# Kernel optimization log

Measured on AMD Instinct MI355X. Metric: run time of the kernel, lower is better.

The kernel has to match this reference:

```python
import jax, jax.numpy as jnp
import numpy as np

N_NODES = 100000
N_EDGES = 1600000
F_IN = 100
HEADS = 3
HEAD_DIM = 64
HIDDEN = HEADS * HEAD_DIM  # 192
NUM_GRAPHS = 128
NUM_CLASSES = 2
NEG_SLOPE_ATT = 0.2   # PyG GATConv attention leaky_relu slope
NEG_SLOPE_ACT = 0.01  # F.leaky_relu default slope


def setup_inputs() -> dict:
    key = jax.random.key(0)
    ks = jax.random.split(key, 9)
    x = jax.random.normal(ks[0], (N_NODES, F_IN), dtype=jnp.float32)
    edge_index = jax.random.randint(ks[1], (2, N_EDGES), 0, N_NODES, dtype=jnp.int64)
    batch = jnp.sort(jax.random.randint(ks[2], (N_NODES,), 0, NUM_GRAPHS, dtype=jnp.int64))
    s = 0.05
    W = jax.random.normal(ks[3], (F_IN, HIDDEN), dtype=jnp.float32) * s
    att_src = jax.random.normal(ks[4], (HEADS, HEAD_DIM), dtype=jnp.float32) * s
    att_dst = jax.random.normal(ks[5], (HEADS, HEAD_DIM), dtype=jnp.float32) * s
    bias = jax.random.normal(ks[6], (HIDDEN,), dtype=jnp.float32) * s
    cls_W = jax.random.normal(ks[7], (HIDDEN, NUM_CLASSES), dtype=jnp.float32) * s
    cls_b = jax.random.normal(ks[8], (NUM_CLASSES,), dtype=jnp.float32) * s
    return {"x": x, "edge_index": edge_index, "batch": batch, "W": W,
            "att_src": att_src, "att_dst": att_dst, "bias": bias,
            "cls_W": cls_W, "cls_b": cls_b}


def _gat_forward(x, edge_index, batch, W, att_src, att_dst, bias, cls_W, cls_b):
    N = x.shape[0]
    # PyG GATConv adds self-loops by default
    loops = jnp.arange(N, dtype=edge_index.dtype)
    src = jnp.concatenate([edge_index[0], loops])
    dst = jnp.concatenate([edge_index[1], loops])

    h = (x @ W).reshape(N, HEADS, HEAD_DIM)          # [N,H,C]
    a_src = jnp.sum(h * att_src, axis=-1)            # [N,H]
    a_dst = jnp.sum(h * att_dst, axis=-1)            # [N,H]

    e = a_src[src] + a_dst[dst]                      # [Etot,H]
    e = jax.nn.leaky_relu(e, NEG_SLOPE_ATT)

    # segment softmax over incoming edges of each destination node
    m = jax.ops.segment_max(e, dst, num_segments=N)  # [N,H]
    e = jnp.exp(e - m[dst])
    denom = jax.ops.segment_sum(e, dst, num_segments=N)
    alpha = e / denom[dst]                           # [Etot,H]

    msg = h[src] * alpha[:, :, None]                 # [Etot,H,C]
    out = jax.ops.segment_sum(msg, dst, num_segments=N).reshape(N, HIDDEN) + bias

    out = jax.nn.leaky_relu(out, NEG_SLOPE_ACT)      # F.leaky_relu (dropout inactive: eval)
    pooled = jax.ops.segment_max(out, batch, num_segments=NUM_GRAPHS)  # global_max_pool
    return pooled @ cls_W + cls_b                    # [NUM_GRAPHS, NUM_CLASSES]


def reference(x, edge_index, batch, W, att_src, att_dst, bias, cls_W, cls_b):
    return _gat_forward(x, edge_index, batch, W, att_src, att_dst, bias, cls_W, cls_b)
```

## Files before the change

kernel.cpp:

```cpp
#include <hip/hip_runtime.h>
#include <math.h>

#define N_NODES   100000
#define N_EDGES   1600000
#define ETOT      1700000
#define F_IN      100
#define HEADS     3
#define HEAD_DIM  64
#define HIDDEN    192
#define NUM_GRAPHS 128
#define NUM_CLASSES 2
#define WT_COLS   208
#define KPAD      128
#define NCHUNK    ((ETOT + 1023) / 1024)
#define DRANGE    (N_NODES / 8)
#define NGEMM     (N_NODES / 32)
#define SCAT_BLKS 2048
#define OSTRIDE   200
#define GAGG      16
#define CAP       64

typedef unsigned short ushort_t;
typedef __attribute__((ext_vector_type(8))) short short8;
typedef __attribute__((ext_vector_type(4))) float floatx4;

__device__ __forceinline__ unsigned f2ord(float f) {
    unsigned u = __float_as_uint(f);
    return (u & 0x80000000u) ? ~u : (u | 0x80000000u);
}
__device__ __forceinline__ float ord2f(unsigned u) {
    return __uint_as_float((u & 0x80000000u) ? (u & 0x7fffffffu) : ~u);
}
__device__ __forceinline__ unsigned bf16rn(float f) {
    unsigned u = __float_as_uint(f);
    return (u + 0x7fffu + ((u >> 16) & 1u)) >> 16;
}
__device__ __forceinline__ int rl_i(int v, int l) {
    return __builtin_amdgcn_readlane(v, l);
}
__device__ __forceinline__ float rl_f(float v, int l) {
    return __uint_as_float((unsigned)__builtin_amdgcn_readlane((int)__float_as_uint(v), l));
}
template<int CTRL>
__device__ __forceinline__ float bfly(float v) {
    int t = __builtin_amdgcn_update_dpp(0, (int)__float_as_uint(v), CTRL, 0xF, 0xF, false);
    return v + __uint_as_float((unsigned)t);
}
#define DPP_XOR1 0xB1
#define DPP_XOR2 0x4E
#define DPP_XOR8 0x128

__global__ __launch_bounds__(256) void k_prep(
        const float* __restrict__ W, const float* __restrict__ att_src,
        const float* __restrict__ att_dst,
        ushort_t* __restrict__ WT_hi, ushort_t* __restrict__ WT_lo) {
    const int c0 = blockIdx.x * 8;
    const int t = threadIdx.x;
    __shared__ float wsv_s[F_IN * 6];
    if (c0 < HIDDEN + 6 && c0 + 8 > HIDDEN) {
        for (int p = t; p < F_IN * 6; p += 256) {
            int k = p / 6, j = p % 6;
            const float* a = (j < 3) ? att_src : att_dst;
            int hh = j % 3;
            float s = 0.f;
            for (int c = 0; c < HEAD_DIM; c++)
                s += W[k * HIDDEN + hh * HEAD_DIM + c] * a[hh * HEAD_DIM + c];
            wsv_s[p] = s;
        }
        __syncthreads();
    }
    for (int idx = t; idx < 8 * KPAD; idx += 256) {
        int col = c0 + (idx >> 7), k = idx & (KPAD - 1);
        float v = 0.f;
        if (k < F_IN) {
            if (col < HIDDEN) v = W[k * HIDDEN + col];
            else if (col < HIDDEN + 6) v = wsv_s[k * 6 + (col - HIDDEN)];
        }
        unsigned hi = bf16rn(v);
        WT_hi[col * KPAD + k] = (ushort_t)hi;
        float lo = v - __uint_as_float(hi << 16);
        WT_lo[col * KPAD + k] = (ushort_t)bf16rn(lo);
    }
}

__global__ __launch_bounds__(256) void k_gemm(
        const float* __restrict__ x,
        const ushort_t* __restrict__ WT_hi, const ushort_t* __restrict__ WT_lo,
        ushort_t* __restrict__ hb,
        float* __restrict__ asrc, float* __restrict__ adst) {
    __shared__ ushort_t lds[32 * 136 * 2];
    const int tid = threadIdx.x;

    ushort_t* xs_hi = lds;
    ushort_t* xs_lo = lds + 32 * 136;
    const int base = blockIdx.x * 32;
    for (int idx = tid; idx < 32 * 14; idx += 256) {
        int row = idx / 14, u = idx % 14;
        *(unsigned*)(xs_hi + row * 136 + 100 + u * 2) = 0u;
        *(unsigned*)(xs_lo + row * 136 + 100 + u * 2) = 0u;
    }
    for (int p = tid; p < 32 * 25; p += 256) {
        int row = p / 25, q = p % 25;
        float4 v = *(const float4*)(x + (size_t)(base + row) * F_IN + q * 4);
        float vv[4] = {v.x, v.y, v.z, v.w};
        ushort_t h4[4], l4[4];
#pragma unroll
        for (int e = 0; e < 4; e++) {
            unsigned hi = bf16rn(vv[e]);
            h4[e] = (ushort_t)hi;
            float lo = vv[e] - __uint_as_float(hi << 16);
            l4[e] = (ushort_t)bf16rn(lo);
        }
        int off = row * 136 + q * 4;
        *(uint2*)(xs_hi + off) = *(uint2*)h4;
        *(uint2*)(xs_lo + off) = *(uint2*)l4;
    }
    __syncthreads();

    const int wid = tid >> 6, l = tid & 63;
    const int row16 = l & 15, g = l >> 4;
    const int NT = (wid == 3) ? 4 : 3;
    const int t0 = wid * 3;

    floatx4 acc[2][4];
#pragma unroll
    for (int m = 0; m < 2; m++)
#pragma unroll
        for (int i = 0; i < 4; i++) acc[m][i] = (floatx4)0.f;

#pragma unroll
    for (int c = 0; c < 4; c++) {
        const int ke = g * 8 + c * 32;
        short8 ah0 = *(const short8*)(xs_hi + row16 * 136 + ke);
        short8 al0 = *(const short8*)(xs_lo + row16 * 136 + ke);
        short8 ah1 = *(const short8*)(xs_hi + (16 + row16) * 136 + ke);
        short8 al1 = *(const short8*)(xs_lo + (16 + row16) * 136 + ke);
#pragma unroll
        for (int ti = 0; ti < 4; ti++) {
            if (ti >= NT) break;
            const int col = (t0 + ti) * 16 + row16;
            short8 bh = *(const short8*)(WT_hi + col * KPAD + ke);
            short8 bl = *(const short8*)(WT_lo + col * KPAD + ke);
            acc[0][ti] = __builtin_amdgcn_mfma_f32_16x16x32_bf16(ah0, bh, acc[0][ti], 0, 0, 0);
            acc[0][ti] = __builtin_amdgcn_mfma_f32_16x16x32_bf16(ah0, bl, acc[0][ti], 0, 0, 0);
            acc[0][ti] = __builtin_amdgcn_mfma_f32_16x16x32_bf16(al0, bh, acc[0][ti], 0, 0, 0);
            acc[1][ti] = __builtin_amdgcn_mfma_f32_16x16x32_bf16(ah1, bh, acc[1][ti], 0, 0, 0);
            acc[1][ti] = __builtin_amdgcn_mfma_f32_16x16x32_bf16(ah1, bl, acc[1][ti], 0, 0, 0);
            acc[1][ti] = __builtin_amdgcn_mfma_f32_16x16x32_bf16(al1, bh, acc[1][ti], 0, 0, 0);
        }
    }

    __syncthreads();

#pragma unroll
    for (int ti = 0; ti < 4; ti++) {
        if (ti >= NT) break;
        const int tile = t0 + ti;
        if (tile < 12) {
#pragma unroll
            for (int m = 0; m < 2; m++)
#pragma unroll
                for (int r = 0; r < 4; r++) {
                    int node = m * 16 + g * 4 + r;
                    lds[node * OSTRIDE + tile * 16 + row16] =
                        (ushort_t)bf16rn(acc[m][ti][r]);
                }
        } else if (row16 < 6) {
#pragma unroll
            for (int m = 0; m < 2; m++)
#pragma unroll
                for (int r = 0; r < 4; r++) {
                    int node = base + m * 16 + g * 4 + r;
                    if (row16 < 3) asrc[node * HEADS + row16] = acc[m][ti][r];
                    else           adst[node * HEADS + (row16 - 3)] = acc[m][ti][r];
                }
        }
    }
    __syncthreads();

    uint4* hb4 = (uint4*)(hb + (size_t)base * HIDDEN);
#pragma unroll
    for (int i = 0; i < 3; i++) {
        int q = tid + i * 256;
        int row = q / 24, c8 = q % 24;
        hb4[q] = *(const uint4*)(lds + row * OSTRIDE + c8 * 8);
    }
}

__global__ __launch_bounds__(256) void k_scat(
        const int* __restrict__ ei, int* __restrict__ count,
        int* __restrict__ srcs) {
    const int tid = threadIdx.x;
    const int s = blockIdx.x;
    const int cls = s & 7;
    const int dlo = cls * DRANGE, dhi = dlo + DRANGE;
    for (int chunk = s >> 3; chunk < NCHUNK; chunk += SCAT_BLKS / 8) {
        const int base = chunk * 1024 + tid;
        int d4[4], s4[4];
#pragma unroll
        for (int q = 0; q < 4; q++) {
            int j = base + q * 256;
            if (j >= ETOT) { d4[q] = -1; s4[q] = 0; continue; }
            d4[q] = (j < N_EDGES) ? ei[N_EDGES + j] : (j - N_EDGES);
            s4[q] = (j < N_EDGES) ? ei[j] : d4[q];
        }
#pragma unroll
        for (int q = 0; q < 4; q++) {
            int d = d4[q];
            if (d < dlo || d >= dhi) continue;
            int pos = atomicAdd(&count[d], 1);
            if (pos < CAP) srcs[d * CAP + pos] = s4[q];
        }
    }
}

__global__ __launch_bounds__(192) void k_aggr(const int* __restrict__ count,
        const int* __restrict__ srcs, const float* __restrict__ asrc,
        const float* __restrict__ adst, const ushort_t* __restrict__ hb,
        const float* __restrict__ bias, const int* __restrict__ batch,
        unsigned* __restrict__ pooled) {
    __shared__ float sm[HIDDEN];
    const int n0 = blockIdx.x * GAGG;
    const int tid = threadIdx.x;
    const int head = tid >> 6, lane = tid & 63;
    const int srci = (lane & 3) | ((lane >> 1) & 4);
    const int slot = ((lane >> 2) & 1) | ((lane >> 3) & 6);
    const char* hbase = (const char*)hb + head * 128 + slot * 16;
    const int c0 = head * HEAD_DIM + slot * 8;

    int cntv = (lane < GAGG) ? count[n0 + lane] : 0;
    int bgv  = (lane < GAGG) ? batch[n0 + lane] : 0;
    float adv = (lane < GAGG * HEADS) ? adst[n0 * HEADS + lane] : 0.f;
    float bv[8];
#pragma unroll
    for (int k = 0; k < 8; k++) bv[k] = bias[c0 + k];

    float vmax[8];
#pragma unroll
    for (int k = 0; k < 8; k++) vmax[k] = -INFINITY;
    int curg = rl_i(bgv, 0);

    int cnt_cur = rl_i(cntv, 0); if (cnt_cur > CAP) cnt_cur = CAP;
    int sA = srcs[(size_t)n0 * CAP + lane];
    int sB = (GAGG > 1) ? srcs[(size_t)(n0 + 1) * CAP + lane] : 0;
    float aA = (lane < cnt_cur) ? asrc[sA * HEADS + head] : 0.f;

    for (int g = 0; g < GAGG; g++) {
        const int gg = rl_i(bgv, g);
        if (gg != curg) {
            if ((lane & 11) == 0) {
#pragma unroll
                for (int k = 0; k < 8; k++) sm[c0 + k] = vmax[k];
            }
            __syncthreads();
            atomicMax(&pooled[curg * HIDDEN + tid], f2ord(sm[tid]));
            __syncthreads();
#pragma unroll
            for (int k = 0; k < 8; k++) vmax[k] = -INFINITY;
            curg = gg;
        }

        const int cnt = cnt_cur;
        const float ad = rl_f(adv, g * HEADS + head);

        int sC = (g + 2 < GAGG) ? srcs[(size_t)(n0 + g + 2) * CAP + lane] : 0;
        int cnt_nxt = 0; float aB = 0.f;
        if (g + 1 < GAGG) {
            cnt_nxt = rl_i(cntv, g + 1); if (cnt_nxt > CAP) cnt_nxt = CAP;
            if (lane < cnt_nxt) aB = asrc[sB * HEADS + head];
        }

        float myexp = 0.f; int myoff = 0;
        if (lane < cnt) {
            float e = aA + ad;
            e = (e > 0.f) ? e : 0.2f * e;
            myexp = __expf(e);
            myoff = sA * (HIDDEN * 2);
        }

        float acc[8];
#pragma unroll
        for (int k = 0; k < 8; k++) acc[k] = 0.f;
        float dpart = 0.f;
        int groups = (cnt + 7) >> 3;
#pragma unroll 2
        for (int j = 0; j < groups; j++) {
            int sl = j * 8 + srci;
            float a   = __shfl(myexp, sl);
            int   off = __shfl(myoff, sl);
            uint4 u = *(const uint4*)(hbase + off);
            acc[0] += a * __uint_as_float(u.x << 16);
            acc[1] += a * __uint_as_float(u.x & 0xffff0000u);
            acc[2] += a * __uint_as_float(u.y << 16);
            acc[3] += a * __uint_as_float(u.y & 0xffff0000u);
            acc[4] += a * __uint_as_float(u.z << 16);
            acc[5] += a * __uint_as_float(u.z & 0xffff0000u);
            acc[6] += a * __uint_as_float(u.w << 16);
            acc[7] += a * __uint_as_float(u.w & 0xffff0000u);
            dpart += a;
        }

        dpart = bfly<DPP_XOR1>(dpart);
        dpart = bfly<DPP_XOR2>(dpart);
        dpart = bfly<DPP_XOR8>(dpart);
#pragma unroll
        for (int k = 0; k < 8; k++) {
            acc[k] = bfly<DPP_XOR1>(acc[k]);
            acc[k] = bfly<DPP_XOR2>(acc[k]);
            acc[k] = bfly<DPP_XOR8>(acc[k]);
        }

        const float inv = 1.f / dpart;
#pragma unroll
        for (int k = 0; k < 8; k++) {
            float v = acc[k] * inv + bv[k];
            v = (v > 0.f) ? v : 0.01f * v;
            vmax[k] = fmaxf(vmax[k], v);
        }

        sA = sB; sB = sC; aA = aB; cnt_cur = cnt_nxt;
    }

    if ((lane & 11) == 0) {
#pragma unroll
        for (int k = 0; k < 8; k++) sm[c0 + k] = vmax[k];
    }
    __syncthreads();
    atomicMax(&pooled[curg * HIDDEN + tid], f2ord(sm[tid]));
}

__global__ __launch_bounds__(64) void k_cls(const unsigned* __restrict__ pooled,
        const float* __restrict__ clsW, const float* __restrict__ clsb,
        float* __restrict__ out) {
    const int g = blockIdx.x, lane = threadIdx.x;
    float s0 = 0.f, s1 = 0.f;
#pragma unroll
    for (int i = 0; i < 3; i++) {
        int f = i * 64 + lane;
        float pv = ord2f(pooled[g * HIDDEN + f]);
        s0 += pv * clsW[f * NUM_CLASSES];
        s1 += pv * clsW[f * NUM_CLASSES + 1];
    }
#pragma unroll
    for (int m = 1; m < 64; m <<= 1) {
        s0 += __shfl_xor(s0, m);
        s1 += __shfl_xor(s1, m);
    }
    if (lane == 0) {
        out[g * NUM_CLASSES]     = s0 + clsb[0];
        out[g * NUM_CLASSES + 1] = s1 + clsb[1];
    }
}

extern "C" void kernel_launch(void* const* d_in, const int* in_sizes, int n_in,
                              void* d_out, int out_size, void* d_ws, size_t ws_size,
                              hipStream_t stream) {
    const float* x       = (const float*)d_in[0];
    const int*   ei      = (const int*)d_in[1];
    const int*   batch   = (const int*)d_in[2];
    const float* W       = (const float*)d_in[3];
    const float* att_src = (const float*)d_in[4];
    const float* att_dst = (const float*)d_in[5];
    const float* bias    = (const float*)d_in[6];
    const float* clsW    = (const float*)d_in[7];
    const float* clsb    = (const float*)d_in[8];
    float* out = (float*)d_out;

    char* p = (char*)d_ws;
    auto alloc = [&](size_t bytes) {
        char* r = p; p += (bytes + 255) & ~size_t(255); return r;
    };
    ushort_t* hb     = (ushort_t*)alloc(sizeof(ushort_t) * N_NODES * HIDDEN);
    float*    asrc   = (float*)   alloc(sizeof(float) * N_NODES * HEADS);
    float*    adst   = (float*)   alloc(sizeof(float) * N_NODES * HEADS);
    int*      count  = (int*)     alloc(sizeof(int) * N_NODES);
    int*      srcs   = (int*)     alloc(sizeof(int) * (size_t)N_NODES * CAP);
    ushort_t* WT_hi  = (ushort_t*)alloc(sizeof(ushort_t) * WT_COLS * KPAD);
    ushort_t* WT_lo  = (ushort_t*)alloc(sizeof(ushort_t) * WT_COLS * KPAD);
    unsigned* pooled = (unsigned*)alloc(sizeof(unsigned) * NUM_GRAPHS * HIDDEN);

    hipMemsetAsync(count, 0, sizeof(int) * N_NODES, stream);
    hipMemsetAsync(pooled, 0, sizeof(unsigned) * NUM_GRAPHS * HIDDEN, stream);

    k_prep<<<WT_COLS / 8, 256, 0, stream>>>(W, att_src, att_dst, WT_hi, WT_lo);
    k_gemm<<<NGEMM, 256, 0, stream>>>(x, WT_hi, WT_lo, hb, asrc, adst);
    k_scat<<<SCAT_BLKS, 256, 0, stream>>>(ei, count, srcs);
    k_aggr<<<N_NODES / GAGG, 192, 0, stream>>>(count, srcs, asrc, adst, hb, bias,
                                               batch, pooled);
    k_cls<<<NUM_GRAPHS, 64, 0, stream>>>(pooled, clsW, clsb, out);
}
```

Measured before the change: 359.1 us.

## Merge edge scatter and GEMM into one launch, batch aggregation gathers

The GEMM and the edge-bucketing scatter are merged into one kernel, with the first blocks doing the scatter and the rest doing the GEMM, so the two independent stages can overlap on the GPU and one launch is saved. Scatter stores and aggregation loads of the source lists now use nontemporal hints to reduce cache pollution. The aggregation inner loop issues up to four gathers before doing the FMAs, exposing more memory-level parallelism. The costs are extra register pressure in the aggregation kernel and the risk that the atomic-heavy scatter blocks contend with the GEMM blocks for resources.

After: 345.7 us. -3.7%, faster.

```diff
diff --git a/kernel.cpp b/kernel.cpp
--- a/kernel.cpp
+++ b/kernel.cpp
@@ -83,17 +83,45 @@
     }
 }
 
-__global__ __launch_bounds__(256) void k_gemm(
+__global__ __launch_bounds__(256) void k_mega(
         const float* __restrict__ x,
         const ushort_t* __restrict__ WT_hi, const ushort_t* __restrict__ WT_lo,
         ushort_t* __restrict__ hb,
-        float* __restrict__ asrc, float* __restrict__ adst) {
+        float* __restrict__ asrc, float* __restrict__ adst,
+        const int* __restrict__ ei, int* __restrict__ count,
+        int* __restrict__ srcs) {
     __shared__ ushort_t lds[32 * 136 * 2];
     const int tid = threadIdx.x;
 
+    if (blockIdx.x < SCAT_BLKS) {
+        const int s = blockIdx.x;
+        const int cls = s & 7;
+        const int dlo = cls * DRANGE, dhi = dlo + DRANGE;
+        for (int chunk = s >> 3; chunk < NCHUNK; chunk += SCAT_BLKS / 8) {
+            const int base = chunk * 1024 + tid;
+            int d4[4], s4[4];
+#pragma unroll
+            for (int q = 0; q < 4; q++) {
+                int j = base + q * 256;
+                if (j >= ETOT) { d4[q] = -1; s4[q] = 0; continue; }
+                d4[q] = (j < N_EDGES) ? ei[N_EDGES + j] : (j - N_EDGES);
+                s4[q] = (j < N_EDGES) ? ei[j] : d4[q];
+            }
+#pragma unroll
+            for (int q = 0; q < 4; q++) {
+                int d = d4[q];
+                if (d < dlo || d >= dhi) continue;
+                int pos = atomicAdd(&count[d], 1);
+                if (pos < CAP)
+                    __builtin_nontemporal_store(s4[q], &srcs[(size_t)d * CAP + pos]);
+            }
+        }
+        return;
+    }
+
     ushort_t* xs_hi = lds;
     ushort_t* xs_lo = lds + 32 * 136;
-    const int base = blockIdx.x * 32;
+    const int base = (blockIdx.x - SCAT_BLKS) * 32;
     for (int idx = tid; idx < 32 * 14; idx += 256) {
         int row = idx / 14, u = idx % 14;
         *(unsigned*)(xs_hi + row * 136 + 100 + u * 2) = 0u;
@@ -187,32 +215,18 @@
     }
 }
 
-__global__ __launch_bounds__(256) void k_scat(
-        const int* __restrict__ ei, int* __restrict__ count,
-        int* __restrict__ srcs) {
-    const int tid = threadIdx.x;
-    const int s = blockIdx.x;
-    const int cls = s & 7;
-    const int dlo = cls * DRANGE, dhi = dlo + DRANGE;
-    for (int chunk = s >> 3; chunk < NCHUNK; chunk += SCAT_BLKS / 8) {
-        const int base = chunk * 1024 + tid;
-        int d4[4], s4[4];
-#pragma unroll
-        for (int q = 0; q < 4; q++) {
-            int j = base + q * 256;
-            if (j >= ETOT) { d4[q] = -1; s4[q] = 0; continue; }
-            d4[q] = (j < N_EDGES) ? ei[N_EDGES + j] : (j - N_EDGES);
-            s4[q] = (j < N_EDGES) ? ei[j] : d4[q];
-        }
-#pragma unroll
-        for (int q = 0; q < 4; q++) {
-            int d = d4[q];
-            if (d < dlo || d >= dhi) continue;
-            int pos = atomicAdd(&count[d], 1);
-            if (pos < CAP) srcs[d * CAP + pos] = s4[q];
-        }
-    }
-}
+#define GAT_FMA(u, a)                                         \
+    do {                                                      \
+        acc[0] += (a) * __uint_as_float((u).x << 16);         \
+        acc[1] += (a) * __uint_as_float((u).x & 0xffff0000u); \
+        acc[2] += (a) * __uint_as_float((u).y << 16);         \
+        acc[3] += (a) * __uint_as_float((u).y & 0xffff0000u); \
+        acc[4] += (a) * __uint_as_float((u).z << 16);         \
+        acc[5] += (a) * __uint_as_float((u).z & 0xffff0000u); \
+        acc[6] += (a) * __uint_as_float((u).w << 16);         \
+        acc[7] += (a) * __uint_as_float((u).w & 0xffff0000u); \
+        dpart += (a);                                         \
+    } while (0)
 
 __global__ __launch_bounds__(192) void k_aggr(const int* __restrict__ count,
         const int* __restrict__ srcs, const float* __restrict__ asrc,
@@ -241,8 +255,8 @@
     int curg = rl_i(bgv, 0);
 
     int cnt_cur = rl_i(cntv, 0); if (cnt_cur > CAP) cnt_cur = CAP;
-    int sA = srcs[(size_t)n0 * CAP + lane];
-    int sB = (GAGG > 1) ? srcs[(size_t)(n0 + 1) * CAP + lane] : 0;
+    int sA = __builtin_nontemporal_load(&srcs[(size_t)n0 * CAP + lane]);
+    int sB = (GAGG > 1) ? __builtin_nontemporal_load(&srcs[(size_t)(n0 + 1) * CAP + lane]) : 0;
     float aA = (lane < cnt_cur) ? asrc[sA * HEADS + head] : 0.f;
 
     for (int g = 0; g < GAGG; g++) {
@@ -263,7 +277,8 @@
         const int cnt = cnt_cur;
         const float ad = rl_f(adv, g * HEADS + head);
 
-        int sC = (g + 2 < GAGG) ? srcs[(size_t)(n0 + g + 2) * CAP + lane] : 0;
+        int sC = (g + 2 < GAGG) ?
+            __builtin_nontemporal_load(&srcs[(size_t)(n0 + g + 2) * CAP + lane]) : 0;
         int cnt_nxt = 0; float aB = 0.f;
         if (g + 1 < GAGG) {
             cnt_nxt = rl_i(cntv, g + 1); if (cnt_nxt > CAP) cnt_nxt = CAP;
@@ -282,22 +297,29 @@
 #pragma unroll
         for (int k = 0; k < 8; k++) acc[k] = 0.f;
         float dpart = 0.f;
-        int groups = (cnt + 7) >> 3;
-#pragma unroll 2
-        for (int j = 0; j < groups; j++) {
+        const int groups = (cnt + 7) >> 3;
+        const int g4 = (groups > 4) ? 4 : groups;
+
+        float av[4]; int ov[4]; uint4 uv[4];
+#pragma unroll
+        for (int j = 0; j < 4; j++) {
+            if (j < g4) {
+                int sl = j * 8 + srci;
+                av[j] = __shfl(myexp, sl);
+                ov[j] = __shfl(myoff, sl);
+                uv[j] = *(const uint4*)(hbase + ov[j]);
+            }
+        }
+#pragma unroll
+        for (int j = 0; j < 4; j++) {
+            if (j < g4) GAT_FMA(uv[j], av[j]);
+        }
+        for (int j = 4; j < groups; j++) {
             int sl = j * 8 + srci;
             float a   = __shfl(myexp, sl);
             int   off = __shfl(myoff, sl);
             uint4 u = *(const uint4*)(hbase + off);
-            acc[0] += a * __uint_as_float(u.x << 16);
-            acc[1] += a * __uint_as_float(u.x & 0xffff0000u);
-            acc[2] += a * __uint_as_float(u.y << 16);
-            acc[3] += a * __uint_as_float(u.y & 0xffff0000u);
-            acc[4] += a * __uint_as_float(u.z << 16);
-            acc[5] += a * __uint_as_float(u.z & 0xffff0000u);
-            acc[6] += a * __uint_as_float(u.w << 16);
-            acc[7] += a * __uint_as_float(u.w & 0xffff0000u);
-            dpart += a;
+            GAT_FMA(u, a);
         }
 
         dpart = bfly<DPP_XOR1>(dpart);
@@ -383,8 +405,8 @@
     hipMemsetAsync(pooled, 0, sizeof(unsigned) * NUM_GRAPHS * HIDDEN, stream);
 
     k_prep<<<WT_COLS / 8, 256, 0, stream>>>(W, att_src, att_dst, WT_hi, WT_lo);
-    k_gemm<<<NGEMM, 256, 0, stream>>>(x, WT_hi, WT_lo, hb, asrc, adst);
-    k_scat<<<SCAT_BLKS, 256, 0, stream>>>(ei, count, srcs);
+    k_mega<<<SCAT_BLKS + NGEMM, 256, 0, stream>>>(x, WT_hi, WT_lo, hb, asrc, adst,
+                                                  ei, count, srcs);
     k_aggr<<<N_NODES / GAGG, 192, 0, stream>>>(count, srcs, asrc, adst, hb, bias,
                                                batch, pooled);
     k_cls<<<NUM_GRAPHS, 64, 0, stream>>>(pooled, clsW, clsb, out);
```
